# Performance work log

Hardware: AMD Instinct MI355X
Metric: run time of the kernel (lower is better)

## Reference

```python
import jax, jax.numpy as jnp
import numpy as np

N = 50000      # num nodes
HID = 64       # hidden_dim
N2V = 64       # node2vec dim
E = 800000     # num edges
EP = 100000    # prediction edges
L = 2          # num_layers
EPS = 1e-5     # BatchNorm eps


def setup_inputs() -> dict:
    key = jax.random.key(0)
    ks = jax.random.split(key, 8)
    edge_index = jax.random.randint(ks[0], (2, E), 0, N)
    pred_edge = jax.random.randint(ks[1], (EP, 2), 0, N)
    id_emb = jax.random.normal(ks[2], (N, HID), jnp.float32) * 0.1      # learnable ID embedding
    n2v_emb = jax.random.normal(ks[3], (N, N2V), jnp.float32) * 0.1     # frozen node2vec embedding
    proj_w = jax.random.normal(ks[4], (HID + N2V, HID), jnp.float32) / np.sqrt(HID + N2V)
    proj_b = jnp.zeros((HID,), jnp.float32)
    conv_w = jax.random.normal(ks[5], (L, HID, HID), jnp.float32) / np.sqrt(HID)
    conv_b = jnp.zeros((L, HID), jnp.float32)
    bn_gamma = jnp.ones((L, HID), jnp.float32)
    bn_beta = jnp.zeros((L, HID), jnp.float32)
    return {"edge_index": edge_index, "pred_edge": pred_edge, "id_emb": id_emb,
            "n2v_emb": n2v_emb, "proj_w": proj_w, "proj_b": proj_b,
            "conv_w": conv_w, "conv_b": conv_b, "bn_gamma": bn_gamma, "bn_beta": bn_beta}


def reference(edge_index, pred_edge, id_emb, n2v_emb, proj_w, proj_b, conv_w, conv_b, bn_gamma, bn_beta):
    # input projection of concatenated embeddings: [N, HID+N2V] @ [HID+N2V, HID]
    x = jnp.concatenate([id_emb, n2v_emb], axis=1) @ proj_w + proj_b

    # GCN normalization with self-loops: norm_e = d^-1/2[src] * d^-1/2[dst]
    loops = jnp.arange(N, dtype=edge_index.dtype)
    row = jnp.concatenate([edge_index[0], loops])   # source nodes
    col = jnp.concatenate([edge_index[1], loops])   # destination nodes
    deg = jax.ops.segment_sum(jnp.ones(row.shape, x.dtype), col, num_segments=N)
    dis = jnp.where(deg > 0, jax.lax.rsqrt(deg), 0.0)
    norm = dis[row] * dis[col]                      # [E+N]

    for l in range(L):
        h = x @ conv_w[l]                                                    # [N, HID]
        agg = jax.ops.segment_sum(norm[:, None] * h[row], col, num_segments=N) + conv_b[l]
        # BatchNorm1d (training-mode batch stats over nodes)
        mu = agg.mean(axis=0)
        var = agg.var(axis=0)
        xn = (agg - mu) * jax.lax.rsqrt(var + EPS) * bn_gamma[l] + bn_beta[l]
        x = x + jax.nn.relu(xn)                                              # residual (shapes match)

    # dot-product link decoder
    z = x
    return (z[pred_edge[:, 0]] * z[pred_edge[:, 1]]).sum(axis=1)
```

## Files before the change

### kernel.cpp

```cpp
#include <hip/hip_runtime.h>

#define NN 50000
#define HID 64
#define NE 800000
#define NP 100000
#define BN_EPS 1e-5f
#define NB1 196

static inline size_t alignup(size_t x) { return (x + 255) & ~(size_t)255; }

__device__ __forceinline__ void f4fma(float a, const float4& w, float4& c) {
    c.x += a * w.x; c.y += a * w.y; c.z += a * w.z; c.w += a * w.w;
}
__device__ __forceinline__ void f4add(const float4& a, float4& c) {
    c.x += a.x; c.y += a.y; c.z += a.z; c.w += a.w;
}
__device__ __forceinline__ unsigned bfpack(float a, float b) {
    unsigned ua = __float_as_uint(a), ub = __float_as_uint(b);
    ua = (ua + 0x7fffu + ((ua >> 16) & 1u)) >> 16;
    ub = (ub + 0x7fffu + ((ub >> 16) & 1u)) >> 16;
    return ua | (ub << 16);
}
__device__ __forceinline__ unsigned short bf1(float a) {
    unsigned ua = __float_as_uint(a);
    return (unsigned short)((ua + 0x7fffu + ((ua >> 16) & 1u)) >> 16);
}
__device__ __forceinline__ float4 bf2f4(uint2 u) {
    float4 r;
    r.x = __uint_as_float(u.x << 16);
    r.y = __uint_as_float(u.x & 0xffff0000u);
    r.z = __uint_as_float(u.y << 16);
    r.w = __uint_as_float(u.y & 0xffff0000u);
    return r;
}


__global__ __launch_bounds__(256) void k_zero(int* __restrict__ cnt, float* __restrict__ sums,
                                              int* __restrict__ cursor) {
    int i = blockIdx.x * blockDim.x + threadIdx.x;
    if (i < NN) cnt[i] = 0;
    if (i < 256) sums[i] = 0.f;
    if (i == 0) *cursor = 0;
}


__global__ __launch_bounds__(256) void k_count(const int* __restrict__ col,
                                               int* __restrict__ cnt, int* __restrict__ rank) {
    int e = blockIdx.x * blockDim.x + threadIdx.x;
    if (e < NE) rank[e] = atomicAdd(&cnt[col[e]], 1);
}


__global__ __launch_bounds__(256) void k_alloc(const int* __restrict__ cnt,
                                               int* __restrict__ offs,
                                               float* __restrict__ dis,
                                               int* __restrict__ cursor) {
    __shared__ int s[256];
    __shared__ int base;
    int t = threadIdx.x;
    int i = blockIdx.x * 256 + t;
    int v = (i < NN) ? cnt[i] : 0;
    if (i < NN) dis[i] = rsqrtf((float)(v + 1));
    s[t] = v;
    __syncthreads();
    for (int off = 1; off < 256; off <<= 1) {
        int add = (t >= off) ? s[t - off] : 0;
        __syncthreads();
        s[t] += add;
        __syncthreads();
    }
    if (t == 255) base = atomicAdd(cursor, s[255]);
    __syncthreads();
    if (i < NN) offs[i] = base + s[t] - v;
}


__global__ __launch_bounds__(256) void k_fill(const int* __restrict__ row, const int* __restrict__ col,
                                              const int* __restrict__ rank, const int* __restrict__ offs,
                                              int* __restrict__ csr_src) {
    int e = blockIdx.x * blockDim.x + threadIdx.x;
    if (e >= NE) return;
    csr_src[offs[col[e]] + rank[e]] = row[e];
}


__global__ __launch_bounds__(256) void k_proj(const float* __restrict__ id_emb,
                                              const float* __restrict__ n2v,
                                              const float* __restrict__ W,
                                              const float* __restrict__ b,
                                              const float* __restrict__ dis,
                                              float* __restrict__ x,
                                              unsigned short* __restrict__ xh) {
    __shared__ unsigned short Wlh[128 * 64];
    __shared__ unsigned short Al[64 * 132];
    int tid = threadIdx.x;
    int node0 = blockIdx.x * 64;
    for (int i = tid; i < 128 * 64; i += 256) Wlh[i] = bf1(W[i]);
    const float2* id2 = (const float2*)id_emb;
    const float2* nv2 = (const float2*)n2v;
#pragma unroll
    for (int it = 0; it < 16; ++it) {
        int i = it * 256 + tid;
        int r = i >> 6, kp = i & 63;
        int n = node0 + r;
        float2 v = make_float2(0.f, 0.f);
        if (n < NN) v = (kp < 32) ? id2[n * 32 + kp] : nv2[n * 32 + (kp - 32)];
        *(unsigned*)&Al[r * 132 + 2 * kp] = bfpack(v.x, v.y);
    }
    __syncthreads();
    int sub = tid >> 4, q = tid & 15;
    const uint2* W2 = (const uint2*)Wlh;
    float4* x4 = (float4*)x;
    uint2* xh2 = (uint2*)xh;
    float4 bb = ((const float4*)b)[q];
    float4 c0 = bb, c1 = bb, c2 = bb, c3 = bb;
#pragma unroll 4
    for (int k4 = 0; k4 < 32; ++k4) {
        float4 w0 = bf2f4(W2[(k4 * 4 + 0) * 16 + q]);
        float4 w1 = bf2f4(W2[(k4 * 4 + 1) * 16 + q]);
        float4 w2 = bf2f4(W2[(k4 * 4 + 2) * 16 + q]);
        float4 w3 = bf2f4(W2[(k4 * 4 + 3) * 16 + q]);
        float4 a0 = bf2f4(*(const uint2*)&Al[(sub * 4 + 0) * 132 + k4 * 4]);
        float4 a1 = bf2f4(*(const uint2*)&Al[(sub * 4 + 1) * 132 + k4 * 4]);
        float4 a2 = bf2f4(*(const uint2*)&Al[(sub * 4 + 2) * 132 + k4 * 4]);
        float4 a3 = bf2f4(*(const uint2*)&Al[(sub * 4 + 3) * 132 + k4 * 4]);
        f4fma(a0.x, w0, c0); f4fma(a0.y, w1, c0); f4fma(a0.z, w2, c0); f4fma(a0.w, w3, c0);
        f4fma(a1.x, w0, c1); f4fma(a1.y, w1, c1); f4fma(a1.z, w2, c1); f4fma(a1.w, w3, c1);
        f4fma(a2.x, w0, c2); f4fma(a2.y, w1, c2); f4fma(a2.z, w2, c2); f4fma(a2.w, w3, c2);
        f4fma(a3.x, w0, c3); f4fma(a3.y, w1, c3); f4fma(a3.z, w2, c3); f4fma(a3.w, w3, c3);
    }
    int n0 = node0 + sub * 4;
    if (n0 + 0 < NN) { float d = dis[n0+0]; x4[(n0+0)*16+q] = c0;
        xh2[(n0+0)*16+q] = make_uint2(bfpack(c0.x*d,c0.y*d), bfpack(c0.z*d,c0.w*d)); }
    if (n0 + 1 < NN) { float d = dis[n0+1]; x4[(n0+1)*16+q] = c1;
        xh2[(n0+1)*16+q] = make_uint2(bfpack(c1.x*d,c1.y*d), bfpack(c1.z*d,c1.w*d)); }
    if (n0 + 2 < NN) { float d = dis[n0+2]; x4[(n0+2)*16+q] = c2;
        xh2[(n0+2)*16+q] = make_uint2(bfpack(c2.x*d,c2.y*d), bfpack(c2.z*d,c2.w*d)); }
    if (n0 + 3 < NN) { float d = dis[n0+3]; x4[(n0+3)*16+q] = c3;
        xh2[(n0+3)*16+q] = make_uint2(bfpack(c3.x*d,c3.y*d), bfpack(c3.z*d,c3.w*d)); }
}


__global__ __launch_bounds__(256) void k_gather(const int* __restrict__ offs,
                                                const int* __restrict__ cnt,
                                                const int* __restrict__ csr_src,
                                                const float* __restrict__ dis,
                                                const unsigned short* __restrict__ xh,
                                                unsigned short* __restrict__ th) {
    int gw = (blockIdx.x * blockDim.x + threadIdx.x) >> 6;
    int lane = threadIdx.x & 63;
    int sub = lane >> 4, q = lane & 15;
    int node = gw * 4 + sub;
    if (node >= NN) return;
    const uint2* xh2 = (const uint2*)xh;
    float4 acc = make_float4(0.f, 0.f, 0.f, 0.f);
    int j = offs[node], j1 = j + cnt[node];
    for (; j + 7 < j1; j += 8) {
        int s0 = csr_src[j],     s1 = csr_src[j + 1], s2 = csr_src[j + 2], s3 = csr_src[j + 3];
        int s4 = csr_src[j + 4], s5 = csr_src[j + 5], s6 = csr_src[j + 6], s7 = csr_src[j + 7];
        uint2 u0 = xh2[s0 * 16 + q];
        uint2 u1 = xh2[s1 * 16 + q];
        uint2 u2 = xh2[s2 * 16 + q];
        uint2 u3 = xh2[s3 * 16 + q];
        uint2 u4 = xh2[s4 * 16 + q];
        uint2 u5 = xh2[s5 * 16 + q];
        uint2 u6 = xh2[s6 * 16 + q];
        uint2 u7 = xh2[s7 * 16 + q];
        f4add(bf2f4(u0), acc); f4add(bf2f4(u1), acc);
        f4add(bf2f4(u2), acc); f4add(bf2f4(u3), acc);
        f4add(bf2f4(u4), acc); f4add(bf2f4(u5), acc);
        f4add(bf2f4(u6), acc); f4add(bf2f4(u7), acc);
    }
    for (; j < j1; ++j) {
        uint2 u0 = xh2[csr_src[j] * 16 + q];
        f4add(bf2f4(u0), acc);
    }
    f4add(bf2f4(xh2[node * 16 + q]), acc);
    float di = dis[node];
    acc.x *= di; acc.y *= di; acc.z *= di; acc.w *= di;
    ((uint2*)th)[node * 16 + q] = make_uint2(bfpack(acc.x, acc.y), bfpack(acc.z, acc.w));
}


__global__ __launch_bounds__(256) void k_gemm_stats(const unsigned short* __restrict__ th,
                                                    const float* __restrict__ W,
                                                    float* __restrict__ agg,
                                                    float* __restrict__ sums) {
    __shared__ float Wl[64 * 64];
    __shared__ float ls0[16][64];
    __shared__ float ls1[16][64];
    int tid = threadIdx.x;
    for (int i = tid; i < 64 * 64; i += 256) Wl[i] = W[i];
    __syncthreads();
    int sub = tid >> 4, q = tid & 15;
    const uint2* t2 = (const uint2*)th;
    const float4* W4 = (const float4*)Wl;
    float4* agg4 = (float4*)agg;
    float4 s1 = make_float4(0.f, 0.f, 0.f, 0.f), s2 = s1;
    const int ngroups = (NN + 63) / 64;
    for (int g = blockIdx.x; g < ngroups; g += gridDim.x) {
        int n0 = g * 64 + sub * 4;
        int r0 = min(n0 + 0, NN - 1), r1 = min(n0 + 1, NN - 1);
        int r2 = min(n0 + 2, NN - 1), r3 = min(n0 + 3, NN - 1);
        float4 c0 = make_float4(0.f,0.f,0.f,0.f), c1 = c0, c2 = c0, c3 = c0;
#pragma unroll 4
        for (int k4 = 0; k4 < 16; ++k4) {
            float4 a0 = bf2f4(t2[r0 * 16 + k4]);
            float4 a1 = bf2f4(t2[r1 * 16 + k4]);
            float4 a2 = bf2f4(t2[r2 * 16 + k4]);
            float4 a3 = bf2f4(t2[r3 * 16 + k4]);
            float4 w0 = W4[(k4 * 4 + 0) * 16 + q];
            float4 w1 = W4[(k4 * 4 + 1) * 16 + q];
            float4 w2 = W4[(k4 * 4 + 2) * 16 + q];
            float4 w3 = W4[(k4 * 4 + 3) * 16 + q];
            f4fma(a0.x, w0, c0); f4fma(a0.y, w1, c0); f4fma(a0.z, w2, c0); f4fma(a0.w, w3, c0);
            f4fma(a1.x, w0, c1); f4fma(a1.y, w1, c1); f4fma(a1.z, w2, c1); f4fma(a1.w, w3, c1);
            f4fma(a2.x, w0, c2); f4fma(a2.y, w1, c2); f4fma(a2.z, w2, c2); f4fma(a2.w, w3, c2);
            f4fma(a3.x, w0, c3); f4fma(a3.y, w1, c3); f4fma(a3.z, w2, c3); f4fma(a3.w, w3, c3);
        }
        if (n0 + 0 < NN) { agg4[(n0 + 0) * 16 + q] = c0;
            s1.x += c0.x; s1.y += c0.y; s1.z += c0.z; s1.w += c0.w;
            s2.x += c0.x*c0.x; s2.y += c0.y*c0.y; s2.z += c0.z*c0.z; s2.w += c0.w*c0.w; }
        if (n0 + 1 < NN) { agg4[(n0 + 1) * 16 + q] = c1;
            s1.x += c1.x; s1.y += c1.y; s1.z += c1.z; s1.w += c1.w;
            s2.x += c1.x*c1.x; s2.y += c1.y*c1.y; s2.z += c1.z*c1.z; s2.w += c1.w*c1.w; }
        if (n0 + 2 < NN) { agg4[(n0 + 2) * 16 + q] = c2;
            s1.x += c2.x; s1.y += c2.y; s1.z += c2.z; s1.w += c2.w;
            s2.x += c2.x*c2.x; s2.y += c2.y*c2.y; s2.z += c2.z*c2.z; s2.w += c2.w*c2.w; }
        if (n0 + 3 < NN) { agg4[(n0 + 3) * 16 + q] = c3;
            s1.x += c3.x; s1.y += c3.y; s1.z += c3.z; s1.w += c3.w;
            s2.x += c3.x*c3.x; s2.y += c3.y*c3.y; s2.z += c3.z*c3.z; s2.w += c3.w*c3.w; }
    }
    ls0[sub][q * 4 + 0] = s1.x; ls0[sub][q * 4 + 1] = s1.y;
    ls0[sub][q * 4 + 2] = s1.z; ls0[sub][q * 4 + 3] = s1.w;
    ls1[sub][q * 4 + 0] = s2.x; ls1[sub][q * 4 + 1] = s2.y;
    ls1[sub][q * 4 + 2] = s2.z; ls1[sub][q * 4 + 3] = s2.w;
    __syncthreads();
    if (tid < 64) {
        float a = 0.f;
#pragma unroll
        for (int r = 0; r < 16; ++r) a += ls0[r][tid];
        atomicAdd(&sums[tid], a);
    } else if (tid < 128) {
        int c = tid - 64;
        float a = 0.f;
#pragma unroll
        for (int r = 0; r < 16; ++r) a += ls1[r][c];
        atomicAdd(&sums[64 + c], a);
    }
}


__global__ __launch_bounds__(256) void k_bnupdate(const float* __restrict__ agg,
                                                  const float* __restrict__ sums,
                                                  const float* __restrict__ gamma,
                                                  const float* __restrict__ beta,
                                                  const float* __restrict__ dis,
                                                  int prescale,
                                                  float* __restrict__ x,
                                                  unsigned short* __restrict__ xh) {
    int i = blockIdx.x * blockDim.x + threadIdx.x;
    if (i >= NN * 16) return;
    int f4 = i & 15;
    const float invn = 1.0f / (float)NN;
    float4 sm = ((const float4*)sums)[f4];
    float4 sq = ((const float4*)(sums + 64))[f4];
    float4 g = ((const float4*)gamma)[f4];
    float4 be = ((const float4*)beta)[f4];
    float4 a = ((const float4*)agg)[i];
    float4 xv = ((const float4*)x)[i];
    float mu, var, rstd, xn;
    mu = sm.x * invn; var = sq.x * invn - mu * mu; rstd = rsqrtf(var + BN_EPS);
    xn = (a.x - mu) * rstd * g.x + be.x; xv.x += fmaxf(xn, 0.f);
    mu = sm.y * invn; var = sq.y * invn - mu * mu; rstd = rsqrtf(var + BN_EPS);
    xn = (a.y - mu) * rstd * g.y + be.y; xv.y += fmaxf(xn, 0.f);
    mu = sm.z * invn; var = sq.z * invn - mu * mu; rstd = rsqrtf(var + BN_EPS);
    xn = (a.z - mu) * rstd * g.z + be.z; xv.z += fmaxf(xn, 0.f);
    mu = sm.w * invn; var = sq.w * invn - mu * mu; rstd = rsqrtf(var + BN_EPS);
    xn = (a.w - mu) * rstd * g.w + be.w; xv.w += fmaxf(xn, 0.f);
    ((float4*)x)[i] = xv;
    float d = prescale ? dis[i >> 4] : 1.0f;
    ((uint2*)xh)[i] = make_uint2(bfpack(xv.x * d, xv.y * d), bfpack(xv.z * d, xv.w * d));
}


__global__ __launch_bounds__(256) void k_decode(const int* __restrict__ pred,
                                                const unsigned short* __restrict__ zh,
                                                float* __restrict__ out) {
    int gw = (blockIdx.x * blockDim.x + threadIdx.x) >> 6;
    int lane = threadIdx.x & 63;
    int sub = lane >> 4, q = lane & 15;
    int p = gw * 4 + sub;
    if (p >= NP) return;
    const uint2* z2 = (const uint2*)zh;
    int a = pred[2 * p], b = pred[2 * p + 1];
    float4 va = bf2f4(z2[a * 16 + q]);
    float4 vb = bf2f4(z2[b * 16 + q]);
    float v = va.x * vb.x + va.y * vb.y + va.z * vb.z + va.w * vb.w;
    v += __shfl_xor(v, 1);
    v += __shfl_xor(v, 2);
    v += __shfl_xor(v, 4);
    v += __shfl_xor(v, 8);
    if (q == 0) out[p] = v;
}

extern "C" void kernel_launch(void* const* d_in, const int* in_sizes, int n_in,
                              void* d_out, int out_size, void* d_ws, size_t ws_size,
                              hipStream_t stream) {
    const int* edge_index = (const int*)d_in[0];
    const int* pred       = (const int*)d_in[1];
    const float* id_emb   = (const float*)d_in[2];
    const float* n2v      = (const float*)d_in[3];
    const float* proj_w   = (const float*)d_in[4];
    const float* proj_b   = (const float*)d_in[5];
    const float* conv_w   = (const float*)d_in[6];
    const float* gamma    = (const float*)d_in[8];
    const float* beta     = (const float*)d_in[9];
    float* out = (float*)d_out;

    char* ws = (char*)d_ws;
    size_t off = 0;
    float* dis   = (float*)(ws + off); off += alignup(NN * 4);
    int* cnt     = (int*)(ws + off);   off += alignup(NN * 4);
    int* offs    = (int*)(ws + off);   off += alignup(NN * 4);
    int* rank    = (int*)(ws + off);   off += alignup((size_t)NE * 4);
    int* cursor  = (int*)(ws + off);   off += alignup(4);
    int* csr_src = (int*)(ws + off);   off += alignup((size_t)NE * 4);
    float* x     = (float*)(ws + off); off += alignup((size_t)NN * 64 * 4);
    float* agg   = (float*)(ws + off); off += alignup((size_t)NN * 64 * 4);
    unsigned short* xh = (unsigned short*)(ws + off); off += alignup((size_t)NN * 64 * 2);
    unsigned short* th = (unsigned short*)(ws + off); off += alignup((size_t)NN * 64 * 2);
    float* sums  = (float*)(ws + off);

    const int* row = edge_index;
    const int* col = edge_index + NE;

    k_zero<<<NB1, 256, 0, stream>>>(cnt, sums, cursor);
    k_count<<<(NE + 255) / 256, 256, 0, stream>>>(col, cnt, rank);
    k_alloc<<<NB1, 256, 0, stream>>>(cnt, offs, dis, cursor);
    k_fill<<<(NE + 255) / 256, 256, 0, stream>>>(row, col, rank, offs, csr_src);

    k_proj<<<(NN + 63) / 64, 256, 0, stream>>>(id_emb, n2v, proj_w, proj_b, dis, x, xh);

    for (int l = 0; l < 2; ++l) {
        k_gather<<<((NN + 3) / 4 * 64 + 255) / 256, 256, 0, stream>>>(offs, cnt, csr_src, dis, xh, th);
        k_gemm_stats<<<512, 256, 0, stream>>>(th, conv_w + l * 64 * 64, agg, sums + l * 128);
        k_bnupdate<<<(NN * 16 + 255) / 256, 256, 0, stream>>>(agg, sums + l * 128, gamma + l * 64,
                                                              beta + l * 64, dis, (l == 0) ? 1 : 0, x, xh);
    }

    k_decode<<<(NP / 4 * 64 + 255) / 256, 256, 0, stream>>>(pred, xh, out);
}
```

Baseline: 211.2 us.

## Store CSR indices as 16-bit padded rows and halve projection tile

CSR source indices are now stored as unsigned 16-bit values, and each node's segment is padded to a multiple of 8 so the gather can fetch eight indices in one 16-byte vector load. This is meant to cut index traffic and load-instruction count in the neighbour gather. The projection kernel now handles 32 nodes per block instead of 64, giving more blocks and lower per-thread register use, and converts the weights with paired loads. Node ids reach 50000, which exceeds the 16-bit range (max 65535 is fine, so it fits); the padding adds some workspace.

Measured after the change: 201.7 us. 1.05x faster.

```diff
diff --git a/kernel.cpp b/kernel.cpp
--- a/kernel.cpp
+++ b/kernel.cpp
@@ -20,10 +20,6 @@
     ua = (ua + 0x7fffu + ((ua >> 16) & 1u)) >> 16;
     ub = (ub + 0x7fffu + ((ub >> 16) & 1u)) >> 16;
     return ua | (ub << 16);
-}
-__device__ __forceinline__ unsigned short bf1(float a) {
-    unsigned ua = __float_as_uint(a);
-    return (unsigned short)((ua + 0x7fffu + ((ua >> 16) & 1u)) >> 16);
 }
 __device__ __forceinline__ float4 bf2f4(uint2 u) {
     float4 r;
@@ -61,7 +57,8 @@
     int i = blockIdx.x * 256 + t;
     int v = (i < NN) ? cnt[i] : 0;
     if (i < NN) dis[i] = rsqrtf((float)(v + 1));
-    s[t] = v;
+    int va = (v + 7) & ~7;
+    s[t] = va;
     __syncthreads();
     for (int off = 1; off < 256; off <<= 1) {
         int add = (t >= off) ? s[t - off] : 0;
@@ -71,16 +68,16 @@
     }
     if (t == 255) base = atomicAdd(cursor, s[255]);
     __syncthreads();
-    if (i < NN) offs[i] = base + s[t] - v;
+    if (i < NN) offs[i] = base + s[t] - va;
 }
 
 
 __global__ __launch_bounds__(256) void k_fill(const int* __restrict__ row, const int* __restrict__ col,
                                               const int* __restrict__ rank, const int* __restrict__ offs,
-                                              int* __restrict__ csr_src) {
+                                              unsigned short* __restrict__ csr) {
     int e = blockIdx.x * blockDim.x + threadIdx.x;
     if (e >= NE) return;
-    csr_src[offs[col[e]] + rank[e]] = row[e];
+    csr[offs[col[e]] + rank[e]] = (unsigned short)row[e];
 }
 
 
@@ -92,14 +89,20 @@
                                               float* __restrict__ x,
                                               unsigned short* __restrict__ xh) {
     __shared__ unsigned short Wlh[128 * 64];
-    __shared__ unsigned short Al[64 * 132];
+    __shared__ unsigned short Al[32 * 132];
     int tid = threadIdx.x;
-    int node0 = blockIdx.x * 64;
-    for (int i = tid; i < 128 * 64; i += 256) Wlh[i] = bf1(W[i]);
+    int node0 = blockIdx.x * 32;
+    const float2* W2f = (const float2*)W;
+#pragma unroll
+    for (int it = 0; it < 16; ++it) {
+        int i = it * 256 + tid;
+        float2 w = W2f[i];
+        *(unsigned*)&Wlh[2 * i] = bfpack(w.x, w.y);
+    }
     const float2* id2 = (const float2*)id_emb;
     const float2* nv2 = (const float2*)n2v;
 #pragma unroll
-    for (int it = 0; it < 16; ++it) {
+    for (int it = 0; it < 8; ++it) {
         int i = it * 256 + tid;
         int r = i >> 6, kp = i & 63;
         int n = node0 + r;
@@ -113,37 +116,29 @@
     float4* x4 = (float4*)x;
     uint2* xh2 = (uint2*)xh;
     float4 bb = ((const float4*)b)[q];
-    float4 c0 = bb, c1 = bb, c2 = bb, c3 = bb;
+    float4 c0 = bb, c1 = bb;
 #pragma unroll 4
     for (int k4 = 0; k4 < 32; ++k4) {
         float4 w0 = bf2f4(W2[(k4 * 4 + 0) * 16 + q]);
         float4 w1 = bf2f4(W2[(k4 * 4 + 1) * 16 + q]);
         float4 w2 = bf2f4(W2[(k4 * 4 + 2) * 16 + q]);
         float4 w3 = bf2f4(W2[(k4 * 4 + 3) * 16 + q]);
-        float4 a0 = bf2f4(*(const uint2*)&Al[(sub * 4 + 0) * 132 + k4 * 4]);
-        float4 a1 = bf2f4(*(const uint2*)&Al[(sub * 4 + 1) * 132 + k4 * 4]);
-        float4 a2 = bf2f4(*(const uint2*)&Al[(sub * 4 + 2) * 132 + k4 * 4]);
-        float4 a3 = bf2f4(*(const uint2*)&Al[(sub * 4 + 3) * 132 + k4 * 4]);
+        float4 a0 = bf2f4(*(const uint2*)&Al[(sub * 2 + 0) * 132 + k4 * 4]);
+        float4 a1 = bf2f4(*(const uint2*)&Al[(sub * 2 + 1) * 132 + k4 * 4]);
         f4fma(a0.x, w0, c0); f4fma(a0.y, w1, c0); f4fma(a0.z, w2, c0); f4fma(a0.w, w3, c0);
         f4fma(a1.x, w0, c1); f4fma(a1.y, w1, c1); f4fma(a1.z, w2, c1); f4fma(a1.w, w3, c1);
-        f4fma(a2.x, w0, c2); f4fma(a2.y, w1, c2); f4fma(a2.z, w2, c2); f4fma(a2.w, w3, c2);
-        f4fma(a3.x, w0, c3); f4fma(a3.y, w1, c3); f4fma(a3.z, w2, c3); f4fma(a3.w, w3, c3);
-    }
-    int n0 = node0 + sub * 4;
+    }
+    int n0 = node0 + sub * 2;
     if (n0 + 0 < NN) { float d = dis[n0+0]; x4[(n0+0)*16+q] = c0;
         xh2[(n0+0)*16+q] = make_uint2(bfpack(c0.x*d,c0.y*d), bfpack(c0.z*d,c0.w*d)); }
     if (n0 + 1 < NN) { float d = dis[n0+1]; x4[(n0+1)*16+q] = c1;
         xh2[(n0+1)*16+q] = make_uint2(bfpack(c1.x*d,c1.y*d), bfpack(c1.z*d,c1.w*d)); }
-    if (n0 + 2 < NN) { float d = dis[n0+2]; x4[(n0+2)*16+q] = c2;
-        xh2[(n0+2)*16+q] = make_uint2(bfpack(c2.x*d,c2.y*d), bfpack(c2.z*d,c2.w*d)); }
-    if (n0 + 3 < NN) { float d = dis[n0+3]; x4[(n0+3)*16+q] = c3;
-        xh2[(n0+3)*16+q] = make_uint2(bfpack(c3.x*d,c3.y*d), bfpack(c3.z*d,c3.w*d)); }
 }
 
 
 __global__ __launch_bounds__(256) void k_gather(const int* __restrict__ offs,
                                                 const int* __restrict__ cnt,
-                                                const int* __restrict__ csr_src,
+                                                const unsigned short* __restrict__ csr,
                                                 const float* __restrict__ dis,
                                                 const unsigned short* __restrict__ xh,
                                                 unsigned short* __restrict__ th) {
@@ -154,10 +149,15 @@
     if (node >= NN) return;
     const uint2* xh2 = (const uint2*)xh;
     float4 acc = make_float4(0.f, 0.f, 0.f, 0.f);
-    int j = offs[node], j1 = j + cnt[node];
-    for (; j + 7 < j1; j += 8) {
-        int s0 = csr_src[j],     s1 = csr_src[j + 1], s2 = csr_src[j + 2], s3 = csr_src[j + 3];
-        int s4 = csr_src[j + 4], s5 = csr_src[j + 5], s6 = csr_src[j + 6], s7 = csr_src[j + 7];
+    const unsigned short* cs = csr + offs[node];
+    int c = cnt[node];
+    int jj = 0;
+    for (; jj + 7 < c; jj += 8) {
+        uint4 s8 = *(const uint4*)(cs + jj);
+        int s0 = s8.x & 0xffff, s1 = s8.x >> 16;
+        int s2 = s8.y & 0xffff, s3 = s8.y >> 16;
+        int s4 = s8.z & 0xffff, s5 = s8.z >> 16;
+        int s6 = s8.w & 0xffff, s7 = s8.w >> 16;
         uint2 u0 = xh2[s0 * 16 + q];
         uint2 u1 = xh2[s1 * 16 + q];
         uint2 u2 = xh2[s2 * 16 + q];
@@ -171,8 +171,8 @@
         f4add(bf2f4(u4), acc); f4add(bf2f4(u5), acc);
         f4add(bf2f4(u6), acc); f4add(bf2f4(u7), acc);
     }
-    for (; j < j1; ++j) {
-        uint2 u0 = xh2[csr_src[j] * 16 + q];
+    for (; jj < c; ++jj) {
+        uint2 u0 = xh2[cs[jj] * 16 + q];
         f4add(bf2f4(u0), acc);
     }
     f4add(bf2f4(xh2[node * 16 + q]), acc);
@@ -325,7 +325,7 @@
     int* offs    = (int*)(ws + off);   off += alignup(NN * 4);
     int* rank    = (int*)(ws + off);   off += alignup((size_t)NE * 4);
     int* cursor  = (int*)(ws + off);   off += alignup(4);
-    int* csr_src = (int*)(ws + off);   off += alignup((size_t)NE * 4);
+    unsigned short* csr = (unsigned short*)(ws + off); off += alignup((size_t)(NE + NN * 8) * 2);
     float* x     = (float*)(ws + off); off += alignup((size_t)NN * 64 * 4);
     float* agg   = (float*)(ws + off); off += alignup((size_t)NN * 64 * 4);
     unsigned short* xh = (unsigned short*)(ws + off); off += alignup((size_t)NN * 64 * 2);
@@ -338,12 +338,12 @@
     k_zero<<<NB1, 256, 0, stream>>>(cnt, sums, cursor);
     k_count<<<(NE + 255) / 256, 256, 0, stream>>>(col, cnt, rank);
     k_alloc<<<NB1, 256, 0, stream>>>(cnt, offs, dis, cursor);
-    k_fill<<<(NE + 255) / 256, 256, 0, stream>>>(row, col, rank, offs, csr_src);
-
-    k_proj<<<(NN + 63) / 64, 256, 0, stream>>>(id_emb, n2v, proj_w, proj_b, dis, x, xh);
+    k_fill<<<(NE + 255) / 256, 256, 0, stream>>>(row, col, rank, offs, csr);
+
+    k_proj<<<(NN + 31) / 32, 256, 0, stream>>>(id_emb, n2v, proj_w, proj_b, dis, x, xh);
 
     for (int l = 0; l < 2; ++l) {
-        k_gather<<<((NN + 3) / 4 * 64 + 255) / 256, 256, 0, stream>>>(offs, cnt, csr_src, dis, xh, th);
+        k_gather<<<((NN + 3) / 4 * 64 + 255) / 256, 256, 0, stream>>>(offs, cnt, csr, dis, xh, th);
         k_gemm_stats<<<512, 256, 0, stream>>>(th, conv_w + l * 64 * 64, agg, sums + l * 128);
         k_bnupdate<<<(NN * 16 + 255) / 256, 256, 0, stream>>>(agg, sums + l * 128, gamma + l * 64,
                                                               beta + l * 64, dis, (l == 0) ? 1 : 0, x, xh);
```
